# Kernel optimization log

Measured on AMD Instinct MI355X. Metric: run time of the kernel, lower is better.

The kernel has to match this reference:

```python
import jax, jax.numpy as jnp
import numpy as np

N = 50000      # nodes
DEG = 12       # in-degree per node
E = N * DEG    # 600000 edges
IN_FEATS = 256
H_FEATS = 128
NUM_LAYERS = 2
BN_EPS = 1e-5
PD_EPS = 1e-6  # torch pairwise_distance eps


def _batch_norm(x):
    # BatchNorm1d(affine=False) in training mode: per-feature batch stats, biased var
    m = x.mean(axis=0)
    v = ((x - m) ** 2).mean(axis=0)
    return (x - m) / jnp.sqrt(v + BN_EPS)


def setup_inputs() -> dict:
    key = jax.random.key(0)
    ks = jax.random.split(key, 6)
    x = jax.random.normal(ks[0], (N, IN_FEATS), dtype=jnp.float32)
    # xavier-uniform-like scales
    s_init = float(np.sqrt(6.0 / (IN_FEATS + H_FEATS)))
    s_h = float(np.sqrt(6.0 / (2 * H_FEATS)))
    W_init = jax.random.uniform(ks[1], (IN_FEATS, H_FEATS), jnp.float32, -s_init, s_init)
    W0 = jax.random.uniform(ks[2], (H_FEATS, H_FEATS), jnp.float32, -s_h, s_h)
    W1 = jax.random.uniform(ks[3], (H_FEATS, H_FEATS), jnp.float32, -s_h, s_h)
    b0 = jnp.zeros((H_FEATS,), jnp.float32)
    b1 = jnp.zeros((H_FEATS,), jnp.float32)
    src = jax.random.randint(ks[4], (E,), 0, N, dtype=jnp.int32)
    dst = jnp.repeat(jnp.arange(N, dtype=jnp.int32), DEG)  # every node has in-degree DEG
    return {"x": x, "W_init": W_init, "W0": W0, "b0": b0, "W1": W1, "b1": b1,
            "src": src, "dst": dst}


def _embed_nodes(x, W_init, Ws, bs, src, dst):
    # h = act(norm(x @ init_weight)); then GraphConv(norm='none') layers
    h = jax.nn.relu(_batch_norm(x @ W_init))
    for W, b in zip(Ws, bs):
        msg = h[src] @ W                       # [E, H]
        agg = jax.ops.segment_sum(msg, dst, num_segments=N)  # sum aggregation
        h = jax.nn.relu(_batch_norm(agg + b))
    return h


def _nonparametric_embedding(x, src, dst, deg):
    # GIN(apply_func=None, eps=-1, aggregator='mean') == mean of in-neighbors
    h = jax.nn.relu(_batch_norm(x))
    for _ in range(NUM_LAYERS):
        agg = jax.ops.segment_sum(h[src], dst, num_segments=N) / deg[:, None]
        h = jax.nn.relu(_batch_norm(agg))
    return h


def _mean_edge_dist(h, src, dst, deg):
    # apply_edges: pairwise_distance(src, dst); pull: scatter-mean onto dst
    d = jnp.linalg.norm(h[src] - h[dst] + PD_EPS, axis=1)  # [E]
    return jax.ops.segment_sum(d, dst, num_segments=N) / deg  # [N]


def reference(x, W_init, W0, b0, W1, b1, src, dst):
    deg = jnp.maximum(
        jax.ops.segment_sum(jnp.ones((E,), jnp.float32), dst, num_segments=N), 1.0)
    h_final = _embed_nodes(x, W_init, (W0, W1), (b0, b1), src, dst)
    # nonparametric target distances (detached in original)
    h_nonpar = _nonparametric_embedding(jax.lax.stop_gradient(x), src, dst, deg)
    d_nonpar = jax.lax.stop_gradient(_mean_edge_dist(h_nonpar, src, dst, deg))
    d_par = _mean_edge_dist(h_final, src, dst, deg)
    loss = jnp.mean((jnp.log(d_par) - jnp.log(d_nonpar)) ** 2)
    return (h_final, loss)
```

## Files before the change

### kernel.cpp

```cpp
#include <hip/hip_runtime.h>
#include <hip/hip_fp16.h>
#include <math.h>

#define DEG 12
#define BN_EPS 1e-5f
#define PD_EPS 1e-6f

using uint = unsigned int;

typedef _Float16 fp16x8 __attribute__((ext_vector_type(8)));
typedef float f32x2 __attribute__((ext_vector_type(2)));
typedef float f32x4 __attribute__((ext_vector_type(4)));

__device__ inline float2 h2f2(uint u) {
  __half2 h; __builtin_memcpy(&h, &u, 4);
  return __half22float2(h);
}
__device__ inline uint f2h2(float a, float b) {
  __half2 h = __floats2half2_rn(a, b);
  uint u; __builtin_memcpy(&u, &h, 4);
  return u;
}
__device__ inline f32x2 q2f_lo(uint u) { return __builtin_amdgcn_cvt_pk_f32_fp8(u, false); }
__device__ inline f32x2 q2f_hi(uint u) { return __builtin_amdgcn_cvt_pk_f32_fp8(u, true); }
__device__ inline uint f4_to_q(float a, float b, float c, float d) {
  uint w = 0;
  w = __builtin_amdgcn_cvt_pk_fp8_f32(a, b, w, false);
  w = __builtin_amdgcn_cvt_pk_fp8_f32(c, d, w, true);
  return w;
}

#define STATS_NB 256

template<int F>
__global__ __launch_bounds__(512) void stats_q_part(const uint* __restrict__ in,
                                                    float* __restrict__ parts, int M) {
  const int G = F / 8;
  __shared__ float redA[512 * 8];
  __shared__ float redB[512 * 8];
  int tid = threadIdx.x;
  int total = M * G;
  float s[8] = {0,0,0,0,0,0,0,0}, q[8] = {0,0,0,0,0,0,0,0};
  for (int i = blockIdx.x * 512 + tid; i < total; i += gridDim.x * 512) {
    uint2 raw = ((const uint2*)in)[i];
    f32x2 a = q2f_lo(raw.x), b = q2f_hi(raw.x), c = q2f_lo(raw.y), d = q2f_hi(raw.y);
    float v[8] = {a.x, a.y, b.x, b.y, c.x, c.y, d.x, d.y};
#pragma unroll
    for (int j = 0; j < 8; ++j) { s[j] += v[j]; q[j] += v[j] * v[j]; }
  }
#pragma unroll
  for (int j = 0; j < 8; ++j) { redA[tid * 8 + j] = s[j]; redB[tid * 8 + j] = q[j]; }
  __syncthreads();
  if (tid < F) {
    int c = tid >> 3, j = tid & 7;
    float as = 0.f, aq = 0.f;
#pragma unroll 4
    for (int r = 0; r < 512 / G; ++r) {
      as += redA[(r * G + c) * 8 + j];
      aq += redB[(r * G + c) * 8 + j];
    }
    parts[blockIdx.x * 2 * F + tid]     = as;
    parts[blockIdx.x * 2 * F + F + tid] = aq;
  }
}

template<int F>
__global__ __launch_bounds__(512) void stats_f_part(const float* __restrict__ in,
                                                    float* __restrict__ parts, int M) {
  const int G = F / 4;
  __shared__ float redA[512 * 4];
  __shared__ float redB[512 * 4];
  int tid = threadIdx.x;
  int total = M * G;
  float s[4] = {0,0,0,0}, q[4] = {0,0,0,0};
  for (int i = blockIdx.x * 512 + tid; i < total; i += gridDim.x * 512) {
    float4 v = ((const float4*)in)[i];
    float w[4] = {v.x, v.y, v.z, v.w};
#pragma unroll
    for (int j = 0; j < 4; ++j) { s[j] += w[j]; q[j] += w[j] * w[j]; }
  }
#pragma unroll
  for (int j = 0; j < 4; ++j) { redA[tid * 4 + j] = s[j]; redB[tid * 4 + j] = q[j]; }
  __syncthreads();
  if (tid < F) {
    int c = tid >> 2, j = tid & 3;
    float as = 0.f, aq = 0.f;
#pragma unroll 4
    for (int r = 0; r < 512 / G; ++r) {
      as += redA[(r * G + c) * 4 + j];
      aq += redB[(r * G + c) * 4 + j];
    }
    parts[blockIdx.x * 2 * F + tid]     = as;
    parts[blockIdx.x * 2 * F + F + tid] = aq;
  }
}

template<int F>
__global__ __launch_bounds__(1024) void stats_final(const float* __restrict__ parts,
                                                    int nb, int M, float* __restrict__ stats) {
  const int OUT = 2 * F;
  const int T   = 1024 / OUT;
  __shared__ float red[1024];
  int tid = threadIdx.x;
  int o = tid & (OUT - 1);
  int c = tid / OUT;
  float s = 0.f;
#pragma unroll 16
  for (int b = c; b < nb; b += T) s += parts[(size_t)b * OUT + o];
  red[tid] = s;
  __syncthreads();
  if (tid < OUT) {
    float acc = red[tid];
#pragma unroll
    for (int cc = 1; cc < T; ++cc) acc += red[cc * OUT + tid];
    red[tid] = acc;
  }
  __syncthreads();
  if (tid < F) {
    float mean = red[tid] / (float)M;
    float var  = red[F + tid] / (float)M - mean * mean;
    stats[tid]     = mean;
    stats[F + tid] = 1.0f / sqrtf(var + BN_EPS);
  }
}

__global__ void transpose_all(const float* __restrict__ Wi, const float* __restrict__ W0,
                              const float* __restrict__ W1, __half* __restrict__ WiT,
                              __half* __restrict__ W0T, __half* __restrict__ W1T) {
  int idx = blockIdx.x * 256 + threadIdx.x;
  if (idx < 32768) {
    int n = idx / 256, k = idx - n * 256;
    WiT[idx] = __float2half(Wi[(size_t)k * 128 + n]);
  } else if (idx < 49152) {
    int i = idx - 32768; int n = i / 128, k = i - n * 128;
    W0T[i] = __float2half(W0[(size_t)k * 128 + n]);
  } else if (idx < 65536) {
    int i = idx - 49152; int n = i / 128, k = i - n * 128;
    W1T[i] = __float2half(W1[(size_t)k * 128 + n]);
  }
}

__device__ __forceinline__ void colstats_epilogue_128(
    void* scratch, const f32x4* acc, int row0w, int M,
    float* __restrict__ parts, int bid, int tid, int kg, int r) {
  float* red = (float*)scratch;
  int slot = (tid >> 6) * 4 + kg;
  __syncthreads();
#pragma unroll
  for (int n = 0; n < 8; ++n) {
    float s = 0.f;
#pragma unroll
    for (int rr = 0; rr < 4; ++rr)
      if (row0w + kg * 4 + rr < M) s += acc[n][rr];
    red[slot * 128 + n * 16 + r] = s;
  }
  __syncthreads();
  if (tid < 128) {
    float s = 0.f;
#pragma unroll
    for (int i = 0; i < 16; ++i) s += red[i * 128 + tid];
    parts[(size_t)bid * 256 + tid] = s;
  }
  __syncthreads();
#pragma unroll
  for (int n = 0; n < 8; ++n) {
    float q = 0.f;
#pragma unroll
    for (int rr = 0; rr < 4; ++rr) {
      float v = (row0w + kg * 4 + rr < M) ? acc[n][rr] : 0.f;
      q += v * v;
    }
    red[slot * 128 + n * 16 + r] = q;
  }
  __syncthreads();
  if (tid < 128) {
    float q = 0.f;
#pragma unroll
    for (int i = 0; i < 16; ++i) q += red[i * 128 + tid];
    parts[(size_t)bid * 256 + 128 + tid] = q;
  }
}

__global__ __launch_bounds__(256) void gemm_x(
    const float* __restrict__ A, const float* __restrict__ stats,
    const __half* __restrict__ WT, __half* __restrict__ C,
    uint* __restrict__ xq, float* __restrict__ parts, int M) {
  __shared__ uint4 Bs4[64 * 32];
  char* Bs = (char*)Bs4;
  int tid = threadIdx.x;
  int wave = tid >> 6, lane = tid & 63;
  int row0 = blockIdx.x * 64 + wave * 16;
  int r = lane & 15, kg = lane >> 4;
  int arow = row0 + r; if (arow >= M) arow = M - 1;
  bool vrow = (row0 + r) < M;
  const float* Ap = A + (size_t)arow * 256 + kg * 8;

  fp16x8 af[8];
#pragma unroll
  for (int a = 0; a < 8; ++a) {
    int c0 = kg * 8 + a * 32;
    float4 lo = *(const float4*)(Ap + a * 32);
    float4 hi = *(const float4*)(Ap + a * 32 + 4);
    af[a][0] = (_Float16)lo.x; af[a][1] = (_Float16)lo.y;
    af[a][2] = (_Float16)lo.z; af[a][3] = (_Float16)lo.w;
    af[a][4] = (_Float16)hi.x; af[a][5] = (_Float16)hi.y;
    af[a][6] = (_Float16)hi.z; af[a][7] = (_Float16)hi.w;
    float4 m0 = *(const float4*)(stats + c0);
    float4 m1 = *(const float4*)(stats + c0 + 4);
    float4 v0 = *(const float4*)(stats + 256 + c0);
    float4 v1 = *(const float4*)(stats + 256 + c0 + 4);
    float w0 = fmaxf((lo.x - m0.x) * v0.x, 0.f);
    float w1 = fmaxf((lo.y - m0.y) * v0.y, 0.f);
    float w2 = fmaxf((lo.z - m0.z) * v0.z, 0.f);
    float w3 = fmaxf((lo.w - m0.w) * v0.w, 0.f);
    float w4 = fmaxf((hi.x - m1.x) * v1.x, 0.f);
    float w5 = fmaxf((hi.y - m1.y) * v1.y, 0.f);
    float w6 = fmaxf((hi.z - m1.z) * v1.z, 0.f);
    float w7 = fmaxf((hi.w - m1.w) * v1.w, 0.f);
    if (vrow) {
      uint2 q; q.x = f4_to_q(w0, w1, w2, w3); q.y = f4_to_q(w4, w5, w6, w7);
      ((uint2*)xq)[(size_t)arow * 32 + (c0 >> 3)] = q;
    }
  }

  f32x4 acc[8];
#pragma unroll
  for (int n = 0; n < 8; ++n) acc[n] = (f32x4){0.f, 0.f, 0.f, 0.f};
  const uint4* Wg = (const uint4*)WT;

#pragma unroll
  for (int ph = 0; ph < 2; ++ph) {
    __syncthreads();
#pragma unroll
    for (int i = 0; i < 8; ++i) {
      int idx = tid + i * 256;
      int rw = idx >> 5, c16 = idx & 31;
      *(uint4*)(Bs + rw * 512 + ((c16 * 16) ^ ((rw & 7) << 4))) = Wg[ph * 2048 + idx];
    }
    __syncthreads();
#pragma unroll
    for (int a = 0; a < 8; ++a) {
#pragma unroll
      for (int n4 = 0; n4 < 4; ++n4) {
        int rw = n4 * 16 + r;
        fp16x8 bf = *(const fp16x8*)(Bs + rw * 512 + ((kg * 16 + a * 64) ^ ((r & 7) << 4)));
        acc[ph * 4 + n4] = __builtin_amdgcn_mfma_f32_16x16x32_f16(af[a], bf, acc[ph * 4 + n4], 0, 0, 0);
      }
    }
  }
#pragma unroll
  for (int n = 0; n < 8; ++n) {
    int col = n * 16 + r;
#pragma unroll
    for (int rr = 0; rr < 4; ++rr) {
      int row = row0 + kg * 4 + rr;
      if (row < M) C[(size_t)row * 128 + col] = __float2half(acc[n][rr]);
    }
  }
  colstats_epilogue_128(Bs, acc, row0, M, parts, blockIdx.x, tid, kg, r);
}

__global__ __launch_bounds__(256) void gemm_128(
    const __half* __restrict__ A, const __half* __restrict__ WT,
    const float* __restrict__ bias, __half* __restrict__ C,
    float* __restrict__ parts, int M) {
  __shared__ uint4 Bs4[128 * 16];
  char* Bs = (char*)Bs4;
  int tid = threadIdx.x;
  const uint4* Wg = (const uint4*)WT;
#pragma unroll
  for (int i = 0; i < 8; ++i) {
    int idx = tid + i * 256;
    int rw = idx >> 4, c16 = idx & 15;
    *(uint4*)(Bs + rw * 256 + ((c16 * 16) ^ ((rw & 7) << 4))) = Wg[idx];
  }
  int wave = tid >> 6, lane = tid & 63;
  int row0 = blockIdx.x * 64 + wave * 16;
  int r = lane & 15, kg = lane >> 4;
  int arow = row0 + r; if (arow >= M) arow = M - 1;
  const _Float16* Ap = (const _Float16*)A + (size_t)arow * 128 + kg * 8;

  fp16x8 af[4];
#pragma unroll
  for (int a = 0; a < 4; ++a) af[a] = *(const fp16x8*)(Ap + a * 32);

  __syncthreads();
  f32x4 acc[8];
#pragma unroll
  for (int n = 0; n < 8; ++n) acc[n] = (f32x4){0.f, 0.f, 0.f, 0.f};
#pragma unroll
  for (int a = 0; a < 4; ++a) {
#pragma unroll
    for (int n = 0; n < 8; ++n) {
      int rw = n * 16 + r;
      fp16x8 bf = *(const fp16x8*)(Bs + rw * 256 + ((kg * 16 + a * 64) ^ ((r & 7) << 4)));
      acc[n] = __builtin_amdgcn_mfma_f32_16x16x32_f16(af[a], bf, acc[n], 0, 0, 0);
    }
  }
#pragma unroll
  for (int n = 0; n < 8; ++n) {
    int col = n * 16 + r;
    float bv = bias[col];
#pragma unroll
    for (int rr = 0; rr < 4; ++rr) {
      acc[n][rr] += bv;
      int row = row0 + kg * 4 + rr;
      if (row < M) C[(size_t)row * 128 + col] = __float2half(acc[n][rr]);
    }
  }
  colstats_epilogue_128(Bs, acc, row0, M, parts, blockIdx.x, tid, kg, r);
}

template<int F, bool BNRELU>
__global__ __launch_bounds__(256) void agg_n(
    const __half* __restrict__ H, const float* __restrict__ stats,
    const int* __restrict__ src, __half* __restrict__ outh,
    float scale, int n_nodes) {
  const int LPN = F / 8;
  const int NPB = 256 / LPN;
  int tid  = threadIdx.x;
  int g    = tid / LPN;
  int lig  = tid % LPN;
  int node = blockIdx.x * NPB + g;
  if (node >= n_nodes) return;
  float m[8], iv[8];
  if (BNRELU) {
#pragma unroll
    for (int j = 0; j < 8; ++j) {
      m[j]  = stats[lig * 8 + j];
      iv[j] = stats[F + lig * 8 + j];
    }
  }
  int lane = tid & 63;
  int grpStart = lane & (63 ^ (LPN - 1));
  int se = 0;
  if ((lane & (LPN - 1)) < DEG) se = src[node * DEG + (lane & (LPN - 1))];

  const uint4* HH = (const uint4*)H;
  float a[8] = {0,0,0,0,0,0,0,0};
#pragma unroll
  for (int e = 0; e < DEG; ++e) {
    int s = __shfl(se, grpStart + e);
    uint4 raw = HH[(size_t)s * LPN + lig];
    float2 v0 = h2f2(raw.x), v1 = h2f2(raw.y), v2 = h2f2(raw.z), v3 = h2f2(raw.w);
    float w[8] = {v0.x, v0.y, v1.x, v1.y, v2.x, v2.y, v3.x, v3.y};
    if (BNRELU) {
#pragma unroll
      for (int j = 0; j < 8; ++j) w[j] = fmaxf((w[j] - m[j]) * iv[j], 0.f);
    }
#pragma unroll
    for (int j = 0; j < 8; ++j) a[j] += w[j];
  }
  uint4 w;
  w.x = f2h2(a[0] * scale, a[1] * scale);
  w.y = f2h2(a[2] * scale, a[3] * scale);
  w.z = f2h2(a[4] * scale, a[5] * scale);
  w.w = f2h2(a[6] * scale, a[7] * scale);
  ((uint4*)outh)[(size_t)node * LPN + lig] = w;
}

template<bool BNRELU>
__global__ __launch_bounds__(256) void agg_q(
    const uint* __restrict__ H, const float* __restrict__ stats,
    const int* __restrict__ src, uint* __restrict__ outq,
    float scale, int n_nodes) {
  const int LPN = 32;
  int tid  = threadIdx.x;
  int g    = tid >> 5;
  int lig  = tid & 31;
  int node = blockIdx.x * 8 + g;
  if (node >= n_nodes) return;
  float m[8], iv[8];
  if (BNRELU) {
#pragma unroll
    for (int j = 0; j < 8; ++j) {
      m[j]  = stats[lig * 8 + j];
      iv[j] = stats[256 + lig * 8 + j];
    }
  }
  int lane = tid & 63;
  int grpStart = lane & 32;
  int se = 0;
  if ((lane & 31) < DEG) se = src[node * DEG + (lane & 31)];

  const uint2* HH = (const uint2*)H;
  float a[8] = {0,0,0,0,0,0,0,0};
#pragma unroll
  for (int e = 0; e < DEG; ++e) {
    int s = __shfl(se, grpStart + e);
    uint2 raw = HH[(size_t)s * 32 + lig];
    f32x2 p0 = q2f_lo(raw.x), p1 = q2f_hi(raw.x), p2 = q2f_lo(raw.y), p3 = q2f_hi(raw.y);
    float w[8] = {p0.x, p0.y, p1.x, p1.y, p2.x, p2.y, p3.x, p3.y};
    if (BNRELU) {
#pragma unroll
      for (int j = 0; j < 8; ++j) w[j] = fmaxf((w[j] - m[j]) * iv[j], 0.f);
    }
#pragma unroll
    for (int j = 0; j < 8; ++j) a[j] += w[j];
  }
  uint2 w;
  w.x = f4_to_q(a[0] * scale, a[1] * scale, a[2] * scale, a[3] * scale);
  w.y = f4_to_q(a[4] * scale, a[5] * scale, a[6] * scale, a[7] * scale);
  ((uint2*)outq)[(size_t)node * 32 + lig] = w;
}

__global__ __launch_bounds__(256) void dist_q128(
    const uint* __restrict__ H, const int* __restrict__ src,
    float* __restrict__ out, int n_nodes) {
  const int LPN = 16;
  int tid  = threadIdx.x;
  int g    = tid >> 4;
  int lig  = tid & 15;
  int node = blockIdx.x * 16 + g;
  if (node >= n_nodes) return;
  int lane = tid & 63;
  int grpStart = lane & 48;
  int se = 0;
  if ((lane & 15) < DEG) se = src[node * DEG + (lane & 15)];

  const uint2* HH = (const uint2*)H;
  uint2 o = HH[(size_t)node * 16 + lig];
  f32x2 p0 = q2f_lo(o.x), p1 = q2f_hi(o.x), p2 = q2f_lo(o.y), p3 = q2f_hi(o.y);
  float oe[8] = {PD_EPS - p0.x, PD_EPS - p0.y, PD_EPS - p1.x, PD_EPS - p1.y,
                 PD_EPS - p2.x, PD_EPS - p2.y, PD_EPS - p3.x, PD_EPS - p3.y};

  float dsum = 0.f;
#pragma unroll
  for (int e = 0; e < DEG; ++e) {
    int s = __shfl(se, grpStart + e);
    uint2 raw = HH[(size_t)s * 16 + lig];
    f32x2 q0 = q2f_lo(raw.x), q1 = q2f_hi(raw.x), q2 = q2f_lo(raw.y), q3 = q2f_hi(raw.y);
    float w[8] = {q0.x, q0.y, q1.x, q1.y, q2.x, q2.y, q3.x, q3.y};
    float sq = 0.f;
#pragma unroll
    for (int j = 0; j < 8; ++j) {
      float d = w[j] + oe[j];
      sq = fmaf(d, d, sq);
    }
#pragma unroll
    for (int mask = 1; mask < LPN; mask <<= 1) sq += __shfl_xor(sq, mask);
    dsum += sqrtf(sq);
  }
  if (lig == 0) out[node] = dsum * (1.0f / (float)DEG);
}

__global__ __launch_bounds__(256) void dist256_loss(
    const uint* __restrict__ H, const int* __restrict__ src,
    const float* __restrict__ dpar, float* __restrict__ lparts, int n_nodes) {
  __shared__ float red[16];
  const int LPN = 16;
  int tid  = threadIdx.x;
  int g    = tid >> 4;
  int lig  = tid & 15;
  int node = blockIdx.x * 16 + g;
  int lane = tid & 63;
  int grpStart = lane & 48;
  int se = 0;
  if ((lane & 15) < DEG) se = src[node * DEG + (lane & 15)];

  const uint2* HH = (const uint2*)H;
  float oe[16];
#pragma unroll
  for (int k = 0; k < 2; ++k) {
    uint2 o = HH[(size_t)node * 32 + lig * 2 + k];
    f32x2 p0 = q2f_lo(o.x), p1 = q2f_hi(o.x), p2 = q2f_lo(o.y), p3 = q2f_hi(o.y);
    oe[k*8+0] = PD_EPS - p0.x; oe[k*8+1] = PD_EPS - p0.y;
    oe[k*8+2] = PD_EPS - p1.x; oe[k*8+3] = PD_EPS - p1.y;
    oe[k*8+4] = PD_EPS - p2.x; oe[k*8+5] = PD_EPS - p2.y;
    oe[k*8+6] = PD_EPS - p3.x; oe[k*8+7] = PD_EPS - p3.y;
  }

  float dsum = 0.f;
#pragma unroll
  for (int e = 0; e < DEG; ++e) {
    int s = __shfl(se, grpStart + e);
    float sq = 0.f;
#pragma unroll
    for (int k = 0; k < 2; ++k) {
      uint2 raw = HH[(size_t)s * 32 + lig * 2 + k];
      f32x2 q0 = q2f_lo(raw.x), q1 = q2f_hi(raw.x), q2 = q2f_lo(raw.y), q3 = q2f_hi(raw.y);
      float w[8] = {q0.x, q0.y, q1.x, q1.y, q2.x, q2.y, q3.x, q3.y};
#pragma unroll
      for (int j = 0; j < 8; ++j) {
        float d = w[j] + oe[k*8+j];
        sq = fmaf(d, d, sq);
      }
    }
#pragma unroll
    for (int mask = 1; mask < LPN; mask <<= 1) sq += __shfl_xor(sq, mask);
    dsum += sqrtf(sq);
  }
  if (lig == 0) {
    float d = dsum * (1.0f / (float)DEG);
    float t = logf(dpar[node]) - logf(d);
    red[g] = t * t;
  }
  __syncthreads();
  if (tid == 0) {
    float s = 0.f;
#pragma unroll
    for (int i = 0; i < 16; ++i) s += red[i];
    lparts[blockIdx.x] = s;
  }
}

template<int F>
__global__ void bnrelu_q2q(const uint* __restrict__ in, const float* __restrict__ stats,
                           uint* __restrict__ out, int total1) {
  for (int idx = blockIdx.x * blockDim.x + threadIdx.x; idx < total1;
       idx += gridDim.x * blockDim.x) {
    uint raw = in[idx];
    int f0 = (idx & (F / 4 - 1)) * 4;
    f32x2 p0 = q2f_lo(raw), p1 = q2f_hi(raw);
    float w0 = fmaxf((p0.x - stats[f0+0]) * stats[F+f0+0], 0.f);
    float w1 = fmaxf((p0.y - stats[f0+1]) * stats[F+f0+1], 0.f);
    float w2 = fmaxf((p1.x - stats[f0+2]) * stats[F+f0+2], 0.f);
    float w3 = fmaxf((p1.y - stats[f0+3]) * stats[F+f0+3], 0.f);
    out[idx] = f4_to_q(w0, w1, w2, w3);
  }
}

template<int F>
__global__ void bnrelu_dual_h(const __half* __restrict__ in, const float* __restrict__ stats,
                              float* __restrict__ outf, uint* __restrict__ outq, int total8) {
  for (int idx = blockIdx.x * blockDim.x + threadIdx.x; idx < total8;
       idx += gridDim.x * blockDim.x) {
    uint4 raw = ((const uint4*)in)[idx];
    int f0 = (idx & (F / 8 - 1)) * 8;
    float2 v0 = h2f2(raw.x), v1 = h2f2(raw.y), v2 = h2f2(raw.z), v3 = h2f2(raw.w);
    float w0 = fmaxf((v0.x - stats[f0+0]) * stats[F+f0+0], 0.f);
    float w1 = fmaxf((v0.y - stats[f0+1]) * stats[F+f0+1], 0.f);
    float w2 = fmaxf((v1.x - stats[f0+2]) * stats[F+f0+2], 0.f);
    float w3 = fmaxf((v1.y - stats[f0+3]) * stats[F+f0+3], 0.f);
    float w4 = fmaxf((v2.x - stats[f0+4]) * stats[F+f0+4], 0.f);
    float w5 = fmaxf((v2.y - stats[f0+5]) * stats[F+f0+5], 0.f);
    float w6 = fmaxf((v3.x - stats[f0+6]) * stats[F+f0+6], 0.f);
    float w7 = fmaxf((v3.y - stats[f0+7]) * stats[F+f0+7], 0.f);
    ((float4*)outf)[idx * 2]     = make_float4(w0, w1, w2, w3);
    ((float4*)outf)[idx * 2 + 1] = make_float4(w4, w5, w6, w7);
    uint2 q; q.x = f4_to_q(w0, w1, w2, w3); q.y = f4_to_q(w4, w5, w6, w7);
    ((uint2*)outq)[idx] = q;
  }
}

__global__ __launch_bounds__(1024) void loss_final(const float* __restrict__ parts, int nb,
                                                   float* __restrict__ out, float inv_n) {
  __shared__ float red[1024];
  int tid = threadIdx.x;
  float s = 0.f;
  for (int i = tid; i < nb; i += 1024) s += parts[i];
  red[tid] = s;
  __syncthreads();
  for (int st = 512; st; st >>= 1) {
    if (tid < st) red[tid] += red[tid + st];
    __syncthreads();
  }
  if (tid == 0) *out = red[0] * inv_n;
}

extern "C" void kernel_launch(void* const* d_in, const int* in_sizes, int n_in,
                              void* d_out, int out_size, void* d_ws, size_t ws_size,
                              hipStream_t stream) {
  const float* x  = (const float*)d_in[0];
  const float* Wi = (const float*)d_in[1];
  const float* W0 = (const float*)d_in[2];
  const float* b0 = (const float*)d_in[3];
  const float* W1 = (const float*)d_in[4];
  const float* b1 = (const float*)d_in[5];
  const int*  src = (const int*)d_in[6];

  const int N = in_sizes[0] / 256;
  float* out = (float*)d_out;

  const int g64 = (N + 63) / 64;

  const size_t NF = (size_t)N * 128;
  float* S1 = (float*)d_ws;
  float* S2 = S1 + NF;
  float* S3 = S2 + NF;
  float* aux = S3 + NF;
  float* dpar   = aux;
  float* parts  = dpar + N;
  float* s_x    = parts + 204800;
  float* s_y0   = s_x + 512;
  float* s_z1   = s_y0 + 256;
  float* s_z2   = s_z1 + 256;
  float* s_a1   = s_z2 + 256;
  float* s_a2   = s_a1 + 512;
  float* lparts = s_a2 + 512;
  __half* WiT   = (__half*)(lparts + 3200);
  __half* W0T   = (__half*)(lparts + 3200 + 16384);
  __half* W1T   = (__half*)(lparts + 3200 + 24576);
  uint*   xq    = (uint*)(lparts + 3200 + 32768);

  __half* y0h = (__half*)S1;
  __half* H0h = (__half*)S2;
  __half* z1h = (__half*)S1;
  __half* H1h = (__half*)S2;
  __half* z2h = (__half*)S3;
  uint* hq   = (uint*)S1;
  uint* A1q  = (uint*)S3;
  uint* A2q  = (uint*)S2;
  uint* A2nq = (uint*)S1;

  const int g128a = N / 16;
  const int gq32  = N / 8;
  const int gq16  = N / 16;

  transpose_all<<<256, 256, 0, stream>>>(Wi, W0, W1, WiT, W0T, W1T);

  stats_f_part<256><<<STATS_NB, 512, 0, stream>>>(x, parts, N);
  stats_final<256><<<1, 1024, 0, stream>>>(parts, STATS_NB, N, s_x);

  gemm_x<<<g64, 256, 0, stream>>>(x, s_x, WiT, y0h, xq, parts, N);
  stats_final<128><<<1, 1024, 0, stream>>>(parts, g64, N, s_y0);
  agg_n<128, true><<<g128a, 256, 0, stream>>>(y0h, s_y0, src, H0h, 1.0f, N);
  gemm_128<<<g64, 256, 0, stream>>>(H0h, W0T, b0, z1h, parts, N);
  stats_final<128><<<1, 1024, 0, stream>>>(parts, g64, N, s_z1);
  agg_n<128, true><<<g128a, 256, 0, stream>>>(z1h, s_z1, src, H1h, 1.0f, N);
  gemm_128<<<g64, 256, 0, stream>>>(H1h, W1T, b1, z2h, parts, N);
  stats_final<128><<<1, 1024, 0, stream>>>(parts, g64, N, s_z2);
  bnrelu_dual_h<128><<<2048, 256, 0, stream>>>(z2h, s_z2, out, hq, N * 16);
  dist_q128<<<gq16, 256, 0, stream>>>(hq, src, dpar, N);

  agg_q<false><<<gq32, 256, 0, stream>>>(xq, nullptr, src, A1q, 1.0f / DEG, N);
  stats_q_part<256><<<STATS_NB, 512, 0, stream>>>(A1q, parts, N);
  stats_final<256><<<1, 1024, 0, stream>>>(parts, STATS_NB, N, s_a1);
  agg_q<true><<<gq32, 256, 0, stream>>>(A1q, s_a1, src, A2q, 1.0f / DEG, N);
  stats_q_part<256><<<STATS_NB, 512, 0, stream>>>(A2q, parts, N);
  stats_final<256><<<1, 1024, 0, stream>>>(parts, STATS_NB, N, s_a2);
  bnrelu_q2q<256><<<2048, 256, 0, stream>>>(A2q, s_a2, A2nq, N * 64);
  dist256_loss<<<gq16, 256, 0, stream>>>(A2nq, src, dpar, lparts, N);

  loss_final<<<1, 1024, 0, stream>>>(lparts, gq16, out + (size_t)N * 128, 1.0f / (float)N);
}
```

Before: 287.0 us.

## Interleave independent GNN branches into combined kernels to cut launch count

Merges work from the parametric and nonparametric branches into shared launches. Different block ranges run different bodies: aggregation plus stats finalization, GEMM plus stats finalization, normalization plus distance. The goal is to cut the number of kernel launches and serial single-block reduction steps, and to let independent work overlap on the GPU. In exchange, block counts are hard-coded for N=50000, workspace buffers are reassigned, and mixed block types may load-imbalance or lower occupancy because of the larger shared memory footprint.

```diff
diff --git a/kernel.cpp b/kernel.cpp
--- a/kernel.cpp
+++ b/kernel.cpp
@@ -30,104 +30,11 @@
   return w;
 }
 
-#define STATS_NB 256
-
-template<int F>
-__global__ __launch_bounds__(512) void stats_q_part(const uint* __restrict__ in,
-                                                    float* __restrict__ parts, int M) {
-  const int G = F / 8;
-  __shared__ float redA[512 * 8];
-  __shared__ float redB[512 * 8];
-  int tid = threadIdx.x;
-  int total = M * G;
-  float s[8] = {0,0,0,0,0,0,0,0}, q[8] = {0,0,0,0,0,0,0,0};
-  for (int i = blockIdx.x * 512 + tid; i < total; i += gridDim.x * 512) {
-    uint2 raw = ((const uint2*)in)[i];
-    f32x2 a = q2f_lo(raw.x), b = q2f_hi(raw.x), c = q2f_lo(raw.y), d = q2f_hi(raw.y);
-    float v[8] = {a.x, a.y, b.x, b.y, c.x, c.y, d.x, d.y};
-#pragma unroll
-    for (int j = 0; j < 8; ++j) { s[j] += v[j]; q[j] += v[j] * v[j]; }
-  }
-#pragma unroll
-  for (int j = 0; j < 8; ++j) { redA[tid * 8 + j] = s[j]; redB[tid * 8 + j] = q[j]; }
-  __syncthreads();
-  if (tid < F) {
-    int c = tid >> 3, j = tid & 7;
-    float as = 0.f, aq = 0.f;
-#pragma unroll 4
-    for (int r = 0; r < 512 / G; ++r) {
-      as += redA[(r * G + c) * 8 + j];
-      aq += redB[(r * G + c) * 8 + j];
-    }
-    parts[blockIdx.x * 2 * F + tid]     = as;
-    parts[blockIdx.x * 2 * F + F + tid] = aq;
-  }
-}
-
-template<int F>
-__global__ __launch_bounds__(512) void stats_f_part(const float* __restrict__ in,
-                                                    float* __restrict__ parts, int M) {
-  const int G = F / 4;
-  __shared__ float redA[512 * 4];
-  __shared__ float redB[512 * 4];
-  int tid = threadIdx.x;
-  int total = M * G;
-  float s[4] = {0,0,0,0}, q[4] = {0,0,0,0};
-  for (int i = blockIdx.x * 512 + tid; i < total; i += gridDim.x * 512) {
-    float4 v = ((const float4*)in)[i];
-    float w[4] = {v.x, v.y, v.z, v.w};
-#pragma unroll
-    for (int j = 0; j < 4; ++j) { s[j] += w[j]; q[j] += w[j] * w[j]; }
-  }
-#pragma unroll
-  for (int j = 0; j < 4; ++j) { redA[tid * 4 + j] = s[j]; redB[tid * 4 + j] = q[j]; }
-  __syncthreads();
-  if (tid < F) {
-    int c = tid >> 2, j = tid & 3;
-    float as = 0.f, aq = 0.f;
-#pragma unroll 4
-    for (int r = 0; r < 512 / G; ++r) {
-      as += redA[(r * G + c) * 4 + j];
-      aq += redB[(r * G + c) * 4 + j];
-    }
-    parts[blockIdx.x * 2 * F + tid]     = as;
-    parts[blockIdx.x * 2 * F + F + tid] = aq;
-  }
-}
-
-template<int F>
-__global__ __launch_bounds__(1024) void stats_final(const float* __restrict__ parts,
-                                                    int nb, int M, float* __restrict__ stats) {
-  const int OUT = 2 * F;
-  const int T   = 1024 / OUT;
-  __shared__ float red[1024];
-  int tid = threadIdx.x;
-  int o = tid & (OUT - 1);
-  int c = tid / OUT;
-  float s = 0.f;
-#pragma unroll 16
-  for (int b = c; b < nb; b += T) s += parts[(size_t)b * OUT + o];
-  red[tid] = s;
-  __syncthreads();
-  if (tid < OUT) {
-    float acc = red[tid];
-#pragma unroll
-    for (int cc = 1; cc < T; ++cc) acc += red[cc * OUT + tid];
-    red[tid] = acc;
-  }
-  __syncthreads();
-  if (tid < F) {
-    float mean = red[tid] / (float)M;
-    float var  = red[F + tid] / (float)M - mean * mean;
-    stats[tid]     = mean;
-    stats[F + tid] = 1.0f / sqrtf(var + BN_EPS);
-  }
-}
-
-__global__ void transpose_all(const float* __restrict__ Wi, const float* __restrict__ W0,
-                              const float* __restrict__ W1, __half* __restrict__ WiT,
-                              __half* __restrict__ W0T, __half* __restrict__ W1T) {
-  int idx = blockIdx.x * 256 + threadIdx.x;
+
+__device__ __forceinline__ void body_transpose(int bid, int tid,
+    const float* Wi, const float* W0, const float* W1,
+    __half* WiT, __half* W0T, __half* W1T) {
+  int idx = bid * 512 + tid;
   if (idx < 32768) {
     int n = idx / 256, k = idx - n * 256;
     WiT[idx] = __float2half(Wi[(size_t)k * 128 + n]);
@@ -140,6 +47,99 @@
   }
 }
 
+__device__ __forceinline__ void body_stats_f256(int sbid, int tid,
+    const float* __restrict__ in, float* __restrict__ parts, int M) {
+  __shared__ float redA[512 * 4];
+  __shared__ float redB[512 * 4];
+  const int G = 64;
+  int total = M * G;
+  float s[4] = {0,0,0,0}, q[4] = {0,0,0,0};
+  for (int i = sbid * 512 + tid; i < total; i += 256 * 512) {
+    float4 v = ((const float4*)in)[i];
+    float w[4] = {v.x, v.y, v.z, v.w};
+#pragma unroll
+    for (int j = 0; j < 4; ++j) { s[j] += w[j]; q[j] += w[j] * w[j]; }
+  }
+#pragma unroll
+  for (int j = 0; j < 4; ++j) { redA[tid * 4 + j] = s[j]; redB[tid * 4 + j] = q[j]; }
+  __syncthreads();
+  if (tid < 256) {
+    int c = tid >> 2, j = tid & 3;
+    float as = 0.f, aq = 0.f;
+#pragma unroll
+    for (int r = 0; r < 8; ++r) {
+      as += redA[(r * 64 + c) * 4 + j];
+      aq += redB[(r * 64 + c) * 4 + j];
+    }
+    parts[(size_t)sbid * 512 + tid]       = as;
+    parts[(size_t)sbid * 512 + 256 + tid] = aq;
+  }
+}
+
+__device__ __forceinline__ void body_stats_q256(int sbid, int tid,
+    const uint* __restrict__ in, float* __restrict__ parts, int M) {
+  __shared__ float redA[512 * 8];
+  __shared__ float redB[512 * 8];
+  const int G = 32;
+  int total = M * G;
+  float s[8] = {0,0,0,0,0,0,0,0}, q[8] = {0,0,0,0,0,0,0,0};
+  for (int i = sbid * 512 + tid; i < total; i += 256 * 512) {
+    uint2 raw = ((const uint2*)in)[i];
+    f32x2 a = q2f_lo(raw.x), b = q2f_hi(raw.x), c = q2f_lo(raw.y), d = q2f_hi(raw.y);
+    float v[8] = {a.x, a.y, b.x, b.y, c.x, c.y, d.x, d.y};
+#pragma unroll
+    for (int j = 0; j < 8; ++j) { s[j] += v[j]; q[j] += v[j] * v[j]; }
+  }
+#pragma unroll
+  for (int j = 0; j < 8; ++j) { redA[tid * 8 + j] = s[j]; redB[tid * 8 + j] = q[j]; }
+  __syncthreads();
+  if (tid < 256) {
+    int c = tid >> 3, j = tid & 7;
+    float as = 0.f, aq = 0.f;
+#pragma unroll
+    for (int r = 0; r < 16; ++r) {
+      as += redA[(r * 32 + c) * 8 + j];
+      aq += redB[(r * 32 + c) * 8 + j];
+    }
+    parts[(size_t)sbid * 512 + tid]       = as;
+    parts[(size_t)sbid * 512 + 256 + tid] = aq;
+  }
+}
+
+__device__ __forceinline__ void body_sfin128_512(int tid,
+    const float* __restrict__ parts, int nb, int M, float* __restrict__ stats) {
+  __shared__ float red[512];
+  int o = tid & 255, c = tid >> 8;
+  float s = 0.f;
+#pragma unroll 8
+  for (int b = c; b < nb; b += 2) s += parts[(size_t)b * 256 + o];
+  red[tid] = s;
+  __syncthreads();
+  if (tid < 256) red[tid] += red[tid + 256];
+  __syncthreads();
+  if (tid < 128) {
+    float sum = red[tid], sq = red[tid + 128];
+    float mean = sum / (float)M;
+    float var  = sq / (float)M - mean * mean;
+    stats[tid]       = mean;
+    stats[128 + tid] = 1.0f / sqrtf(var + BN_EPS);
+  }
+}
+
+__device__ __forceinline__ void body_sfin256_256(int tid,
+    const float* __restrict__ parts, int nb, int M, float* __restrict__ stats) {
+  float s = 0.f, q = 0.f;
+#pragma unroll 8
+  for (int b = 0; b < nb; ++b) {
+    s += parts[(size_t)b * 512 + tid];
+    q += parts[(size_t)b * 512 + 256 + tid];
+  }
+  float mean = s / (float)M;
+  float var  = q / (float)M - mean * mean;
+  stats[tid]       = mean;
+  stats[256 + tid] = 1.0f / sqrtf(var + BN_EPS);
+}
+
 __device__ __forceinline__ void colstats_epilogue_128(
     void* scratch, const f32x4* acc, int row0w, int M,
     float* __restrict__ parts, int bid, int tid, int kg, int r) {
@@ -178,6 +178,240 @@
 #pragma unroll
     for (int i = 0; i < 16; ++i) q += red[i * 128 + tid];
     parts[(size_t)bid * 256 + 128 + tid] = q;
+  }
+}
+
+__device__ __forceinline__ void body_gemm128(int bid, int tid,
+    const __half* __restrict__ A, const __half* __restrict__ WT,
+    const float* __restrict__ bias, __half* __restrict__ C,
+    float* __restrict__ parts, int M) {
+  __shared__ uint4 Bs4[128 * 16];
+  char* Bs = (char*)Bs4;
+  const uint4* Wg = (const uint4*)WT;
+#pragma unroll
+  for (int i = 0; i < 8; ++i) {
+    int idx = tid + i * 256;
+    int rw = idx >> 4, c16 = idx & 15;
+    *(uint4*)(Bs + rw * 256 + ((c16 * 16) ^ ((rw & 7) << 4))) = Wg[idx];
+  }
+  int wave = tid >> 6, lane = tid & 63;
+  int row0 = bid * 64 + wave * 16;
+  int r = lane & 15, kg = lane >> 4;
+  int arow = row0 + r; if (arow >= M) arow = M - 1;
+  const _Float16* Ap = (const _Float16*)A + (size_t)arow * 128 + kg * 8;
+
+  fp16x8 af[4];
+#pragma unroll
+  for (int a = 0; a < 4; ++a) af[a] = *(const fp16x8*)(Ap + a * 32);
+
+  __syncthreads();
+  f32x4 acc[8];
+#pragma unroll
+  for (int n = 0; n < 8; ++n) acc[n] = (f32x4){0.f, 0.f, 0.f, 0.f};
+#pragma unroll
+  for (int a = 0; a < 4; ++a) {
+#pragma unroll
+    for (int n = 0; n < 8; ++n) {
+      int rw = n * 16 + r;
+      fp16x8 bf = *(const fp16x8*)(Bs + rw * 256 + ((kg * 16 + a * 64) ^ ((r & 7) << 4)));
+      acc[n] = __builtin_amdgcn_mfma_f32_16x16x32_f16(af[a], bf, acc[n], 0, 0, 0);
+    }
+  }
+#pragma unroll
+  for (int n = 0; n < 8; ++n) {
+    int col = n * 16 + r;
+    float bv = bias[col];
+#pragma unroll
+    for (int rr = 0; rr < 4; ++rr) {
+      acc[n][rr] += bv;
+      int row = row0 + kg * 4 + rr;
+      if (row < M) C[(size_t)row * 128 + col] = __float2half(acc[n][rr]);
+    }
+  }
+  colstats_epilogue_128(Bs, acc, row0, M, parts, bid, tid, kg, r);
+}
+
+__device__ __forceinline__ void body_agg_n128(int bid, int tid,
+    const __half* __restrict__ H, const float* __restrict__ stats,
+    const int* __restrict__ src, __half* __restrict__ outh, int n_nodes) {
+  int g = tid >> 4, lig = tid & 15;
+  int node = bid * 32 + g;
+  if (node >= n_nodes) return;
+  float m[8], iv[8];
+#pragma unroll
+  for (int j = 0; j < 8; ++j) {
+    m[j]  = stats[lig * 8 + j];
+    iv[j] = stats[128 + lig * 8 + j];
+  }
+  int lane = tid & 63;
+  int grpStart = lane & 48;
+  int se = 0;
+  if ((lane & 15) < DEG) se = src[node * DEG + (lane & 15)];
+
+  const uint4* HH = (const uint4*)H;
+  float a[8] = {0,0,0,0,0,0,0,0};
+#pragma unroll
+  for (int e = 0; e < DEG; ++e) {
+    int s = __shfl(se, grpStart + e);
+    uint4 raw = HH[(size_t)s * 16 + lig];
+    float2 v0 = h2f2(raw.x), v1 = h2f2(raw.y), v2 = h2f2(raw.z), v3 = h2f2(raw.w);
+    float w[8] = {v0.x, v0.y, v1.x, v1.y, v2.x, v2.y, v3.x, v3.y};
+#pragma unroll
+    for (int j = 0; j < 8; ++j) a[j] += fmaxf((w[j] - m[j]) * iv[j], 0.f);
+  }
+  uint4 w;
+  w.x = f2h2(a[0], a[1]); w.y = f2h2(a[2], a[3]);
+  w.z = f2h2(a[4], a[5]); w.w = f2h2(a[6], a[7]);
+  ((uint4*)outh)[(size_t)node * 16 + lig] = w;
+}
+
+template<bool BN>
+__device__ __forceinline__ void body_agg_q(int bid, int tid,
+    const uint* __restrict__ H, const float* __restrict__ stats,
+    const int* __restrict__ src, uint* __restrict__ outq, float scale) {
+  int g = tid >> 5, lig = tid & 31;
+  int node = bid * 16 + g;
+  float m[8], iv[8];
+  if (BN) {
+#pragma unroll
+    for (int j = 0; j < 8; ++j) {
+      m[j]  = stats[lig * 8 + j];
+      iv[j] = stats[256 + lig * 8 + j];
+    }
+  }
+  int lane = tid & 63;
+  int grpStart = lane & 32;
+  int se = 0;
+  if ((lane & 31) < DEG) se = src[node * DEG + (lane & 31)];
+
+  const uint2* HH = (const uint2*)H;
+  float a[8] = {0,0,0,0,0,0,0,0};
+#pragma unroll
+  for (int e = 0; e < DEG; ++e) {
+    int s = __shfl(se, grpStart + e);
+    uint2 raw = HH[(size_t)s * 32 + lig];
+    f32x2 p0 = q2f_lo(raw.x), p1 = q2f_hi(raw.x), p2 = q2f_lo(raw.y), p3 = q2f_hi(raw.y);
+    float w[8] = {p0.x, p0.y, p1.x, p1.y, p2.x, p2.y, p3.x, p3.y};
+    if (BN) {
+#pragma unroll
+      for (int j = 0; j < 8; ++j) w[j] = fmaxf((w[j] - m[j]) * iv[j], 0.f);
+    }
+#pragma unroll
+    for (int j = 0; j < 8; ++j) a[j] += w[j];
+  }
+  uint2 w;
+  w.x = f4_to_q(a[0] * scale, a[1] * scale, a[2] * scale, a[3] * scale);
+  w.y = f4_to_q(a[4] * scale, a[5] * scale, a[6] * scale, a[7] * scale);
+  ((uint2*)outq)[(size_t)node * 32 + lig] = w;
+}
+
+__device__ __forceinline__ void body_bnq(int bid, int tid,
+    const uint* __restrict__ in, const float* __restrict__ stats,
+    uint* __restrict__ out, int total1) {
+  for (int idx = bid * 512 + tid; idx < total1; idx += 1024 * 512) {
+    uint raw = in[idx];
+    int f0 = (idx & 63) * 4;
+    f32x2 p0 = q2f_lo(raw), p1 = q2f_hi(raw);
+    float w0 = fmaxf((p0.x - stats[f0+0]) * stats[256+f0+0], 0.f);
+    float w1 = fmaxf((p0.y - stats[f0+1]) * stats[256+f0+1], 0.f);
+    float w2 = fmaxf((p1.x - stats[f0+2]) * stats[256+f0+2], 0.f);
+    float w3 = fmaxf((p1.y - stats[f0+3]) * stats[256+f0+3], 0.f);
+    out[idx] = f4_to_q(w0, w1, w2, w3);
+  }
+}
+
+__device__ __forceinline__ void body_bndual(int bid, int tid,
+    const __half* __restrict__ in, const float* __restrict__ stats,
+    float* __restrict__ outf, uint* __restrict__ outq, int total8) {
+  for (int idx = bid * 256 + tid; idx < total8; idx += 2048 * 256) {
+    uint4 raw = ((const uint4*)in)[idx];
+    int f0 = (idx & 15) * 8;
+    float2 v0 = h2f2(raw.x), v1 = h2f2(raw.y), v2 = h2f2(raw.z), v3 = h2f2(raw.w);
+    float w0 = fmaxf((v0.x - stats[f0+0]) * stats[128+f0+0], 0.f);
+    float w1 = fmaxf((v0.y - stats[f0+1]) * stats[128+f0+1], 0.f);
+    float w2 = fmaxf((v1.x - stats[f0+2]) * stats[128+f0+2], 0.f);
+    float w3 = fmaxf((v1.y - stats[f0+3]) * stats[128+f0+3], 0.f);
+    float w4 = fmaxf((v2.x - stats[f0+4]) * stats[128+f0+4], 0.f);
+    float w5 = fmaxf((v2.y - stats[f0+5]) * stats[128+f0+5], 0.f);
+    float w6 = fmaxf((v3.x - stats[f0+6]) * stats[128+f0+6], 0.f);
+    float w7 = fmaxf((v3.y - stats[f0+7]) * stats[128+f0+7], 0.f);
+    ((float4*)outf)[idx * 2]     = make_float4(w0, w1, w2, w3);
+    ((float4*)outf)[idx * 2 + 1] = make_float4(w4, w5, w6, w7);
+    uint2 q; q.x = f4_to_q(w0, w1, w2, w3); q.y = f4_to_q(w4, w5, w6, w7);
+    ((uint2*)outq)[idx] = q;
+  }
+}
+
+__device__ __forceinline__ void body_dist256(int bid, int tid,
+    const uint* __restrict__ H, const int* __restrict__ src,
+    float* __restrict__ dnp) {
+  int g = tid >> 4, lig = tid & 15;
+  int node = bid * 16 + g;
+  int lane = tid & 63;
+  int grpStart = lane & 48;
+  int se = 0;
+  if ((lane & 15) < DEG) se = src[node * DEG + (lane & 15)];
+
+  const uint2* HH = (const uint2*)H;
+  float oe[16];
+#pragma unroll
+  for (int k = 0; k < 2; ++k) {
+    uint2 o = HH[(size_t)node * 32 + lig * 2 + k];
+    f32x2 p0 = q2f_lo(o.x), p1 = q2f_hi(o.x), p2 = q2f_lo(o.y), p3 = q2f_hi(o.y);
+    oe[k*8+0] = PD_EPS - p0.x; oe[k*8+1] = PD_EPS - p0.y;
+    oe[k*8+2] = PD_EPS - p1.x; oe[k*8+3] = PD_EPS - p1.y;
+    oe[k*8+4] = PD_EPS - p2.x; oe[k*8+5] = PD_EPS - p2.y;
+    oe[k*8+6] = PD_EPS - p3.x; oe[k*8+7] = PD_EPS - p3.y;
+  }
+  float dsum = 0.f;
+#pragma unroll
+  for (int e = 0; e < DEG; ++e) {
+    int s = __shfl(se, grpStart + e);
+    float sq = 0.f;
+#pragma unroll
+    for (int k = 0; k < 2; ++k) {
+      uint2 raw = HH[(size_t)s * 32 + lig * 2 + k];
+      f32x2 q0 = q2f_lo(raw.x), q1 = q2f_hi(raw.x), q2 = q2f_lo(raw.y), q3 = q2f_hi(raw.y);
+      float w[8] = {q0.x, q0.y, q1.x, q1.y, q2.x, q2.y, q3.x, q3.y};
+#pragma unroll
+      for (int j = 0; j < 8; ++j) {
+        float d = w[j] + oe[k*8+j];
+        sq = fmaf(d, d, sq);
+      }
+    }
+#pragma unroll
+    for (int mask = 1; mask < 16; mask <<= 1) sq += __shfl_xor(sq, mask);
+    dsum += sqrtf(sq);
+  }
+  if (lig == 0) dnp[node] = dsum * (1.0f / (float)DEG);
+}
+
+
+__global__ __launch_bounds__(512) void k_prep(
+    const float* Wi, const float* W0, const float* W1,
+    __half* WiT, __half* W0T, __half* W1T,
+    const float* x, float* partsB, int M) {
+  if (blockIdx.x < 128) body_transpose(blockIdx.x, threadIdx.x, Wi, W0, W1, WiT, W0T, W1T);
+  else body_stats_f256(blockIdx.x - 128, threadIdx.x, x, partsB, M);
+}
+
+__global__ __launch_bounds__(1024) void k_sfin_x(const float* __restrict__ parts,
+                                                 int nb, int M, float* __restrict__ stats) {
+  __shared__ float red[1024];
+  int tid = threadIdx.x;
+  int o = tid & 511, c = tid >> 9;
+  float s = 0.f;
+#pragma unroll 16
+  for (int b = c; b < nb; b += 2) s += parts[(size_t)b * 512 + o];
+  red[tid] = s;
+  __syncthreads();
+  if (tid < 512) red[tid] += red[tid + 512];
+  __syncthreads();
+  if (tid < 256) {
+    float mean = red[tid] / (float)M;
+    float var  = red[256 + tid] / (float)M - mean * mean;
+    stats[tid]       = mean;
+    stats[256 + tid] = 1.0f / sqrtf(var + BN_EPS);
   }
 }
 
@@ -260,159 +494,49 @@
   colstats_epilogue_128(Bs, acc, row0, M, parts, blockIdx.x, tid, kg, r);
 }
 
-__global__ __launch_bounds__(256) void gemm_128(
-    const __half* __restrict__ A, const __half* __restrict__ WT,
-    const float* __restrict__ bias, __half* __restrict__ C,
-    float* __restrict__ parts, int M) {
-  __shared__ uint4 Bs4[128 * 16];
-  char* Bs = (char*)Bs4;
+template<bool BN>
+__global__ __launch_bounds__(512) void k_aggq_sfin128(
+    const uint* H, const float* astats, const int* src, uint* outq, float scale,
+    const float* partsA, int nb, int M, float* ostats) {
+  if (blockIdx.x < 3125) body_agg_q<BN>(blockIdx.x, threadIdx.x, H, astats, src, outq, scale);
+  else body_sfin128_512(threadIdx.x, partsA, nb, M, ostats);
+}
+
+__global__ __launch_bounds__(512) void k_aggn_statsq(
+    const __half* H, const float* nstats, const int* src, __half* outh, int n,
+    const uint* qin, float* partsB) {
+  if (blockIdx.x < 1563) body_agg_n128(blockIdx.x, threadIdx.x, H, nstats, src, outh, n);
+  else body_stats_q256(blockIdx.x - 1563, threadIdx.x, qin, partsB, n);
+}
+
+__global__ __launch_bounds__(256) void k_gemm_sfin256(
+    const __half* A, const __half* WT, const float* bias, __half* C,
+    float* partsA, int M, const float* partsB, int nb, float* ostats) {
+  if (blockIdx.x < 782) body_gemm128(blockIdx.x, threadIdx.x, A, WT, bias, C, partsA, M);
+  else body_sfin256_256(threadIdx.x, partsB, nb, M, ostats);
+}
+
+__global__ __launch_bounds__(512) void k_bnq_sfin128(
+    const uint* in, const float* stats, uint* outq, int total1,
+    const float* partsA, int nb, int M, float* ostats) {
+  if (blockIdx.x < 1024) body_bnq(blockIdx.x, threadIdx.x, in, stats, outq, total1);
+  else body_sfin128_512(threadIdx.x, partsA, nb, M, ostats);
+}
+
+__global__ __launch_bounds__(256) void k_bndual_dist256(
+    const __half* z2h, const float* stats, float* outf, uint* hq, int total8,
+    const uint* A2nq, const int* src, float* dnp) {
+  if (blockIdx.x < 2048) body_bndual(blockIdx.x, threadIdx.x, z2h, stats, outf, hq, total8);
+  else body_dist256(blockIdx.x - 2048, threadIdx.x, A2nq, src, dnp);
+}
+
+__global__ __launch_bounds__(256) void k_dist128_loss(
+    const uint* __restrict__ H, const int* __restrict__ src,
+    const float* __restrict__ dnp, float* __restrict__ lparts) {
+  __shared__ float red[16];
   int tid = threadIdx.x;
-  const uint4* Wg = (const uint4*)WT;
-#pragma unroll
-  for (int i = 0; i < 8; ++i) {
-    int idx = tid + i * 256;
-    int rw = idx >> 4, c16 = idx & 15;
-    *(uint4*)(Bs + rw * 256 + ((c16 * 16) ^ ((rw & 7) << 4))) = Wg[idx];
-  }
-  int wave = tid >> 6, lane = tid & 63;
-  int row0 = blockIdx.x * 64 + wave * 16;
-  int r = lane & 15, kg = lane >> 4;
-  int arow = row0 + r; if (arow >= M) arow = M - 1;
-  const _Float16* Ap = (const _Float16*)A + (size_t)arow * 128 + kg * 8;
-
-  fp16x8 af[4];
-#pragma unroll
-  for (int a = 0; a < 4; ++a) af[a] = *(const fp16x8*)(Ap + a * 32);
-
-  __syncthreads();
-  f32x4 acc[8];
-#pragma unroll
-  for (int n = 0; n < 8; ++n) acc[n] = (f32x4){0.f, 0.f, 0.f, 0.f};
-#pragma unroll
-  for (int a = 0; a < 4; ++a) {
-#pragma unroll
-    for (int n = 0; n < 8; ++n) {
-      int rw = n * 16 + r;
-      fp16x8 bf = *(const fp16x8*)(Bs + rw * 256 + ((kg * 16 + a * 64) ^ ((r & 7) << 4)));
-      acc[n] = __builtin_amdgcn_mfma_f32_16x16x32_f16(af[a], bf, acc[n], 0, 0, 0);
-    }
-  }
-#pragma unroll
-  for (int n = 0; n < 8; ++n) {
-    int col = n * 16 + r;
-    float bv = bias[col];
-#pragma unroll
-    for (int rr = 0; rr < 4; ++rr) {
-      acc[n][rr] += bv;
-      int row = row0 + kg * 4 + rr;
-      if (row < M) C[(size_t)row * 128 + col] = __float2half(acc[n][rr]);
-    }
-  }
-  colstats_epilogue_128(Bs, acc, row0, M, parts, blockIdx.x, tid, kg, r);
-}
-
-template<int F, bool BNRELU>
-__global__ __launch_bounds__(256) void agg_n(
-    const __half* __restrict__ H, const float* __restrict__ stats,
-    const int* __restrict__ src, __half* __restrict__ outh,
-    float scale, int n_nodes) {
-  const int LPN = F / 8;
-  const int NPB = 256 / LPN;
-  int tid  = threadIdx.x;
-  int g    = tid / LPN;
-  int lig  = tid % LPN;
-  int node = blockIdx.x * NPB + g;
-  if (node >= n_nodes) return;
-  float m[8], iv[8];
-  if (BNRELU) {
-#pragma unroll
-    for (int j = 0; j < 8; ++j) {
-      m[j]  = stats[lig * 8 + j];
-      iv[j] = stats[F + lig * 8 + j];
-    }
-  }
-  int lane = tid & 63;
-  int grpStart = lane & (63 ^ (LPN - 1));
-  int se = 0;
-  if ((lane & (LPN - 1)) < DEG) se = src[node * DEG + (lane & (LPN - 1))];
-
-  const uint4* HH = (const uint4*)H;
-  float a[8] = {0,0,0,0,0,0,0,0};
-#pragma unroll
-  for (int e = 0; e < DEG; ++e) {
-    int s = __shfl(se, grpStart + e);
-    uint4 raw = HH[(size_t)s * LPN + lig];
-    float2 v0 = h2f2(raw.x), v1 = h2f2(raw.y), v2 = h2f2(raw.z), v3 = h2f2(raw.w);
-    float w[8] = {v0.x, v0.y, v1.x, v1.y, v2.x, v2.y, v3.x, v3.y};
-    if (BNRELU) {
-#pragma unroll
-      for (int j = 0; j < 8; ++j) w[j] = fmaxf((w[j] - m[j]) * iv[j], 0.f);
-    }
-#pragma unroll
-    for (int j = 0; j < 8; ++j) a[j] += w[j];
-  }
-  uint4 w;
-  w.x = f2h2(a[0] * scale, a[1] * scale);
-  w.y = f2h2(a[2] * scale, a[3] * scale);
-  w.z = f2h2(a[4] * scale, a[5] * scale);
-  w.w = f2h2(a[6] * scale, a[7] * scale);
-  ((uint4*)outh)[(size_t)node * LPN + lig] = w;
-}
-
-template<bool BNRELU>
-__global__ __launch_bounds__(256) void agg_q(
-    const uint* __restrict__ H, const float* __restrict__ stats,
-    const int* __restrict__ src, uint* __restrict__ outq,
-    float scale, int n_nodes) {
-  const int LPN = 32;
-  int tid  = threadIdx.x;
-  int g    = tid >> 5;
-  int lig  = tid & 31;
-  int node = blockIdx.x * 8 + g;
-  if (node >= n_nodes) return;
-  float m[8], iv[8];
-  if (BNRELU) {
-#pragma unroll
-    for (int j = 0; j < 8; ++j) {
-      m[j]  = stats[lig * 8 + j];
-      iv[j] = stats[256 + lig * 8 + j];
-    }
-  }
-  int lane = tid & 63;
-  int grpStart = lane & 32;
-  int se = 0;
-  if ((lane & 31) < DEG) se = src[node * DEG + (lane & 31)];
-
-  const uint2* HH = (const uint2*)H;
-  float a[8] = {0,0,0,0,0,0,0,0};
-#pragma unroll
-  for (int e = 0; e < DEG; ++e) {
-    int s = __shfl(se, grpStart + e);
-    uint2 raw = HH[(size_t)s * 32 + lig];
-    f32x2 p0 = q2f_lo(raw.x), p1 = q2f_hi(raw.x), p2 = q2f_lo(raw.y), p3 = q2f_hi(raw.y);
-    float w[8] = {p0.x, p0.y, p1.x, p1.y, p2.x, p2.y, p3.x, p3.y};
-    if (BNRELU) {
-#pragma unroll
-      for (int j = 0; j < 8; ++j) w[j] = fmaxf((w[j] - m[j]) * iv[j], 0.f);
-    }
-#pragma unroll
-    for (int j = 0; j < 8; ++j) a[j] += w[j];
-  }
-  uint2 w;
-  w.x = f4_to_q(a[0] * scale, a[1] * scale, a[2] * scale, a[3] * scale);
-  w.y = f4_to_q(a[4] * scale, a[5] * scale, a[6] * scale, a[7] * scale);
-  ((uint2*)outq)[(size_t)node * 32 + lig] = w;
-}
-
-__global__ __launch_bounds__(256) void dist_q128(
-    const uint* __restrict__ H, const int* __restrict__ src,
-    float* __restrict__ out, int n_nodes) {
-  const int LPN = 16;
-  int tid  = threadIdx.x;
-  int g    = tid >> 4;
-  int lig  = tid & 15;
+  int g = tid >> 4, lig = tid & 15;
   int node = blockIdx.x * 16 + g;
-  if (node >= n_nodes) return;
   int lane = tid & 63;
   int grpStart = lane & 48;
   int se = 0;
@@ -438,61 +562,12 @@
       sq = fmaf(d, d, sq);
     }
 #pragma unroll
-    for (int mask = 1; mask < LPN; mask <<= 1) sq += __shfl_xor(sq, mask);
+    for (int mask = 1; mask < 16; mask <<= 1) sq += __shfl_xor(sq, mask);
     dsum += sqrtf(sq);
   }
-  if (lig == 0) out[node] = dsum * (1.0f / (float)DEG);
-}
-
-__global__ __launch_bounds__(256) void dist256_loss(
-    const uint* __restrict__ H, const int* __restrict__ src,
-    const float* __restrict__ dpar, float* __restrict__ lparts, int n_nodes) {
-  __shared__ float red[16];
-  const int LPN = 16;
-  int tid  = threadIdx.x;
-  int g    = tid >> 4;
-  int lig  = tid & 15;
-  int node = blockIdx.x * 16 + g;
-  int lane = tid & 63;
-  int grpStart = lane & 48;
-  int se = 0;
-  if ((lane & 15) < DEG) se = src[node * DEG + (lane & 15)];
-
-  const uint2* HH = (const uint2*)H;
-  float oe[16];
-#pragma unroll
-  for (int k = 0; k < 2; ++k) {
-    uint2 o = HH[(size_t)node * 32 + lig * 2 + k];
-    f32x2 p0 = q2f_lo(o.x), p1 = q2f_hi(o.x), p2 = q2f_lo(o.y), p3 = q2f_hi(o.y);
-    oe[k*8+0] = PD_EPS - p0.x; oe[k*8+1] = PD_EPS - p0.y;
-    oe[k*8+2] = PD_EPS - p1.x; oe[k*8+3] = PD_EPS - p1.y;
-    oe[k*8+4] = PD_EPS - p2.x; oe[k*8+5] = PD_EPS - p2.y;
-    oe[k*8+6] = PD_EPS - p3.x; oe[k*8+7] = PD_EPS - p3.y;
-  }
-
-  float dsum = 0.f;
-#pragma unroll
-  for (int e = 0; e < DEG; ++e) {
-    int s = __shfl(se, grpStart + e);
-    float sq = 0.f;
-#pragma unroll
-    for (int k = 0; k < 2; ++k) {
-      uint2 raw = HH[(size_t)s * 32 + lig * 2 + k];
-      f32x2 q0 = q2f_lo(raw.x), q1 = q2f_hi(raw.x), q2 = q2f_lo(raw.y), q3 = q2f_hi(raw.y);
-      float w[8] = {q0.x, q0.y, q1.x, q1.y, q2.x, q2.y, q3.x, q3.y};
-#pragma unroll
-      for (int j = 0; j < 8; ++j) {
-        float d = w[j] + oe[k*8+j];
-        sq = fmaf(d, d, sq);
-      }
-    }
-#pragma unroll
-    for (int mask = 1; mask < LPN; mask <<= 1) sq += __shfl_xor(sq, mask);
-    dsum += sqrtf(sq);
-  }
   if (lig == 0) {
-    float d = dsum * (1.0f / (float)DEG);
-    float t = logf(dpar[node]) - logf(d);
+    float dpar = dsum * (1.0f / (float)DEG);
+    float t = logf(dpar) - logf(dnp[node]);
     red[g] = t * t;
   }
   __syncthreads();
@@ -504,47 +579,8 @@
   }
 }
 
-template<int F>
-__global__ void bnrelu_q2q(const uint* __restrict__ in, const float* __restrict__ stats,
-                           uint* __restrict__ out, int total1) {
-  for (int idx = blockIdx.x * blockDim.x + threadIdx.x; idx < total1;
-       idx += gridDim.x * blockDim.x) {
-    uint raw = in[idx];
-    int f0 = (idx & (F / 4 - 1)) * 4;
-    f32x2 p0 = q2f_lo(raw), p1 = q2f_hi(raw);
-    float w0 = fmaxf((p0.x - stats[f0+0]) * stats[F+f0+0], 0.f);
-    float w1 = fmaxf((p0.y - stats[f0+1]) * stats[F+f0+1], 0.f);
-    float w2 = fmaxf((p1.x - stats[f0+2]) * stats[F+f0+2], 0.f);
-    float w3 = fmaxf((p1.y - stats[f0+3]) * stats[F+f0+3], 0.f);
-    out[idx] = f4_to_q(w0, w1, w2, w3);
-  }
-}
-
-template<int F>
-__global__ void bnrelu_dual_h(const __half* __restrict__ in, const float* __restrict__ stats,
-                              float* __restrict__ outf, uint* __restrict__ outq, int total8) {
-  for (int idx = blockIdx.x * blockDim.x + threadIdx.x; idx < total8;
-       idx += gridDim.x * blockDim.x) {
-    uint4 raw = ((const uint4*)in)[idx];
-    int f0 = (idx & (F / 8 - 1)) * 8;
-    float2 v0 = h2f2(raw.x), v1 = h2f2(raw.y), v2 = h2f2(raw.z), v3 = h2f2(raw.w);
-    float w0 = fmaxf((v0.x - stats[f0+0]) * stats[F+f0+0], 0.f);
-    float w1 = fmaxf((v0.y - stats[f0+1]) * stats[F+f0+1], 0.f);
-    float w2 = fmaxf((v1.x - stats[f0+2]) * stats[F+f0+2], 0.f);
-    float w3 = fmaxf((v1.y - stats[f0+3]) * stats[F+f0+3], 0.f);
-    float w4 = fmaxf((v2.x - stats[f0+4]) * stats[F+f0+4], 0.f);
-    float w5 = fmaxf((v2.y - stats[f0+5]) * stats[F+f0+5], 0.f);
-    float w6 = fmaxf((v3.x - stats[f0+6]) * stats[F+f0+6], 0.f);
-    float w7 = fmaxf((v3.y - stats[f0+7]) * stats[F+f0+7], 0.f);
-    ((float4*)outf)[idx * 2]     = make_float4(w0, w1, w2, w3);
-    ((float4*)outf)[idx * 2 + 1] = make_float4(w4, w5, w6, w7);
-    uint2 q; q.x = f4_to_q(w0, w1, w2, w3); q.y = f4_to_q(w4, w5, w6, w7);
-    ((uint2*)outq)[idx] = q;
-  }
-}
-
-__global__ __launch_bounds__(1024) void loss_final(const float* __restrict__ parts, int nb,
-                                                   float* __restrict__ out, float inv_n) {
+__global__ __launch_bounds__(1024) void k_loss_final(const float* __restrict__ parts, int nb,
+                                                     float* __restrict__ out, float inv_n) {
   __shared__ float red[1024];
   int tid = threadIdx.x;
   float s = 0.f;
@@ -572,65 +608,47 @@
   const int N = in_sizes[0] / 256;
   float* out = (float*)d_out;
 
-  const int g64 = (N + 63) / 64;
-
-  const size_t NF = (size_t)N * 128;
-  float* S1 = (float*)d_ws;
-  float* S2 = S1 + NF;
-  float* S3 = S2 + NF;
-  float* aux = S3 + NF;
-  float* dpar   = aux;
-  float* parts  = dpar + N;
-  float* s_x    = parts + 204800;
+  float* R1 = (float*)d_ws;
+  float* R2 = R1 + (size_t)N * 64;
+  float* R3 = R2 + (size_t)N * 64;
+  float* R4 = R3 + (size_t)N * 64;
+  float* hqf    = R4 + (size_t)N * 64;
+  float* dnp    = hqf + (size_t)N * 32;
+  float* partsA = dnp + N;
+  float* partsB = partsA + 200192;
+  float* s_x    = partsB + 131072;
   float* s_y0   = s_x + 512;
   float* s_z1   = s_y0 + 256;
   float* s_z2   = s_z1 + 256;
   float* s_a1   = s_z2 + 256;
   float* s_a2   = s_a1 + 512;
   float* lparts = s_a2 + 512;
-  __half* WiT   = (__half*)(lparts + 3200);
-  __half* W0T   = (__half*)(lparts + 3200 + 16384);
-  __half* W1T   = (__half*)(lparts + 3200 + 24576);
-  uint*   xq    = (uint*)(lparts + 3200 + 32768);
-
-  __half* y0h = (__half*)S1;
-  __half* H0h = (__half*)S2;
-  __half* z1h = (__half*)S1;
-  __half* H1h = (__half*)S2;
-  __half* z2h = (__half*)S3;
-  uint* hq   = (uint*)S1;
-  uint* A1q  = (uint*)S3;
-  uint* A2q  = (uint*)S2;
-  uint* A2nq = (uint*)S1;
-
-  const int g128a = N / 16;
-  const int gq32  = N / 8;
-  const int gq16  = N / 16;
-
-  transpose_all<<<256, 256, 0, stream>>>(Wi, W0, W1, WiT, W0T, W1T);
-
-  stats_f_part<256><<<STATS_NB, 512, 0, stream>>>(x, parts, N);
-  stats_final<256><<<1, 1024, 0, stream>>>(parts, STATS_NB, N, s_x);
-
-  gemm_x<<<g64, 256, 0, stream>>>(x, s_x, WiT, y0h, xq, parts, N);
-  stats_final<128><<<1, 1024, 0, stream>>>(parts, g64, N, s_y0);
-  agg_n<128, true><<<g128a, 256, 0, stream>>>(y0h, s_y0, src, H0h, 1.0f, N);
-  gemm_128<<<g64, 256, 0, stream>>>(H0h, W0T, b0, z1h, parts, N);
-  stats_final<128><<<1, 1024, 0, stream>>>(parts, g64, N, s_z1);
-  agg_n<128, true><<<g128a, 256, 0, stream>>>(z1h, s_z1, src, H1h, 1.0f, N);
-  gemm_128<<<g64, 256, 0, stream>>>(H1h, W1T, b1, z2h, parts, N);
-  stats_final<128><<<1, 1024, 0, stream>>>(parts, g64, N, s_z2);
-  bnrelu_dual_h<128><<<2048, 256, 0, stream>>>(z2h, s_z2, out, hq, N * 16);
-  dist_q128<<<gq16, 256, 0, stream>>>(hq, src, dpar, N);
-
-  agg_q<false><<<gq32, 256, 0, stream>>>(xq, nullptr, src, A1q, 1.0f / DEG, N);
-  stats_q_part<256><<<STATS_NB, 512, 0, stream>>>(A1q, parts, N);
-  stats_final<256><<<1, 1024, 0, stream>>>(parts, STATS_NB, N, s_a1);
-  agg_q<true><<<gq32, 256, 0, stream>>>(A1q, s_a1, src, A2q, 1.0f / DEG, N);
-  stats_q_part<256><<<STATS_NB, 512, 0, stream>>>(A2q, parts, N);
-  stats_final<256><<<1, 1024, 0, stream>>>(parts, STATS_NB, N, s_a2);
-  bnrelu_q2q<256><<<2048, 256, 0, stream>>>(A2q, s_a2, A2nq, N * 64);
-  dist256_loss<<<gq16, 256, 0, stream>>>(A2nq, src, dpar, lparts, N);
-
-  loss_final<<<1, 1024, 0, stream>>>(lparts, gq16, out + (size_t)N * 128, 1.0f / (float)N);
-}
+  float* wbase  = lparts + 3200;
+  __half* WiT = (__half*)wbase;
+  __half* W0T = (__half*)(wbase + 16384);
+  __half* W1T = (__half*)(wbase + 16384 + 8192);
+
+  __half* y0h = (__half*)R1;  __half* H1h = (__half*)R1;
+  uint*   xq  = (uint*)R2;    __half* z1h = (__half*)R2;  uint* A2nq = (uint*)R2;
+  uint*   A1q = (uint*)R3;    __half* z2h = (__half*)R3;
+  __half* H0h = (__half*)R4;  uint*   A2q = (uint*)R4;
+  uint*   hq  = (uint*)hqf;
+
+  const int g64 = (N + 63) / 64;
+
+  k_prep<<<384, 512, 0, stream>>>(Wi, W0, W1, WiT, W0T, W1T, x, partsB, N);
+  k_sfin_x<<<1, 1024, 0, stream>>>(partsB, 256, N, s_x);
+  gemm_x<<<g64, 256, 0, stream>>>(x, s_x, WiT, y0h, xq, partsA, N);
+  k_aggq_sfin128<false><<<3126, 512, 0, stream>>>(xq, nullptr, src, A1q, 1.0f / DEG,
+                                                  partsA, g64, N, s_y0);
+  k_aggn_statsq<<<1819, 512, 0, stream>>>(y0h, s_y0, src, H0h, N, A1q, partsB);
+  k_gemm_sfin256<<<783, 256, 0, stream>>>(H0h, W0T, b0, z1h, partsA, N, partsB, 256, s_a1);
+  k_aggq_sfin128<true><<<3126, 512, 0, stream>>>(A1q, s_a1, src, A2q, 1.0f / DEG,
+                                                 partsA, g64, N, s_z1);
+  k_aggn_statsq<<<1819, 512, 0, stream>>>(z1h, s_z1, src, H1h, N, A2q, partsB);
+  k_gemm_sfin256<<<783, 256, 0, stream>>>(H1h, W1T, b1, z2h, partsA, N, partsB, 256, s_a2);
+  k_bnq_sfin128<<<1025, 512, 0, stream>>>(A2q, s_a2, A2nq, N * 64, partsA, g64, N, s_z2);
+  k_bndual_dist256<<<5173, 256, 0, stream>>>(z2h, s_z2, out, hq, N * 16, A2nq, src, dnp);
+  k_dist128_loss<<<3125, 256, 0, stream>>>(hq, src, dnp, lparts);
+  k_loss_final<<<1, 1024, 0, stream>>>(lparts, 3125, out + (size_t)N * 128, 1.0f / (float)N);
+}
```

Measured after the change: 293.0 us. 1.02x slower.
